# Performance work log

Measured on AMD Instinct MI355X. Metric: run time of the kernel, lower is better.

## Reference

```python
import jax, jax.numpy as jnp
import numpy as np

L = 8192
E = 1024
H = 16
D = E // H  # head_dim = 64


def setup_inputs() -> dict:
    key = jax.random.key(0)
    ks = jax.random.split(key, 5)
    x = jax.random.normal(ks[0], (L, E), dtype=jnp.float32)
    in_proj_weight = jax.random.normal(ks[1], (3 * E, E), dtype=jnp.float32) * (1.0 / np.sqrt(E))
    in_proj_bias = jax.random.normal(ks[2], (3 * E,), dtype=jnp.float32) * 0.02
    out_proj_weight = jax.random.normal(ks[3], (E, E), dtype=jnp.float32) * (1.0 / np.sqrt(E))
    out_proj_bias = jax.random.normal(ks[4], (E,), dtype=jnp.float32) * 0.02
    return {
        "x": x,
        "in_proj_weight": in_proj_weight,
        "in_proj_bias": in_proj_bias,
        "out_proj_weight": out_proj_weight,
        "out_proj_bias": out_proj_bias,
    }


def reference(x, in_proj_weight, in_proj_bias, out_proj_weight, out_proj_bias):
    # Single-token query (decode-style): q from x[:1], k/v from full sequence.
    q = x[:1] @ in_proj_weight[:E].T + in_proj_bias[:E]            # [1, E]
    k = x @ in_proj_weight[E:2 * E].T + in_proj_bias[E:2 * E]      # [L, E]
    v = x @ in_proj_weight[2 * E:].T + in_proj_bias[2 * E:]        # [L, E]

    q = q.reshape(1, H, D).transpose(1, 0, 2)   # [H, 1, D]
    k = k.reshape(L, H, D).transpose(1, 2, 0)   # [H, D, L]
    v = v.reshape(L, H, D).transpose(1, 0, 2)   # [H, L, D]

    scale = 1.0 / np.sqrt(D).astype(np.float32)
    dot = jnp.matmul(q, k) * scale              # [H, 1, L]
    attn = jax.nn.softmax(dot, axis=-1)
    out = jnp.matmul(attn, v)                   # [H, 1, D]
    out = out.transpose(1, 0, 2).reshape(1, E)  # [1, E]
    return out @ out_proj_weight.T + out_proj_bias
```

## Files before the change

### kernel.cpp

```cpp
#include <hip/hip_runtime.h>

#define LSEQ 8192
#define E 1024
#define H 16

typedef __attribute__((ext_vector_type(8))) short short8;
typedef __attribute__((ext_vector_type(4))) float f32x4;

__device__ inline unsigned short f2bf(float f) {
    union { float f; unsigned int i; } v; v.f = f;
    unsigned int x = v.i;
    return (unsigned short)((x + 0x7fffu + ((x >> 16) & 1u)) >> 16);
}

__device__ inline float wave_reduce_sum(float v) {
    #pragma unroll
    for (int off = 32; off > 0; off >>= 1) v += __shfl_xor(v, off, 64);
    return v;
}

__global__ __launch_bounds__(256) void k0_q(
    const float* __restrict__ x, const float* __restrict__ W,
    const float* __restrict__ bias, float* __restrict__ q_ws,
    float* __restrict__ S_ws)
{
    if (blockIdx.x == 0 && threadIdx.x < 16) S_ws[threadIdx.x] = 0.f;
    int wave = threadIdx.x >> 6, lane = threadIdx.x & 63;
    int i = blockIdx.x * 4 + wave;
    const f32x4* wp = (const f32x4*)(W + i * E) + lane * 4;
    const f32x4* xp = (const f32x4*)(x) + lane * 4;
    float s = 0.f;
    #pragma unroll
    for (int j = 0; j < 4; j++) {
        f32x4 w4 = wp[j], x4 = xp[j];
        s += w4[0]*x4[0] + w4[1]*x4[1] + w4[2]*x4[2] + w4[3]*x4[3];
    }
    s = wave_reduce_sum(s);
    if (lane == 0) q_ws[i] = s + bias[i];
}

__global__ __launch_bounds__(256) void k1_rc(
    const float* __restrict__ W, const float* __restrict__ bias,
    const float* __restrict__ q_ws, unsigned short* __restrict__ r_bf,
    float* __restrict__ c_ws)
{
    __shared__ float red[4][64];
    int hb = blockIdx.x >> 4, ec = blockIdx.x & 15;
    int lane = threadIdx.x & 63, wq = threadIdx.x >> 6;
    int e = ec * 64 + lane;
    const float* qh = q_ws + hb * 64;
    float acc = 0.f;
    #pragma unroll
    for (int i = 0; i < 16; i++) {
        int d = wq * 16 + i;
        acc += qh[d] * W[(E + hb * 64 + d) * E + e];
    }
    red[wq][lane] = acc;
    __syncthreads();
    if (wq == 0) {
        float s = red[0][lane] + red[1][lane] + red[2][lane] + red[3][lane];
        r_bf[hb * E + e] = f2bf(s * 0.125f);
    }
    if (ec == 0 && wq == 1) {
        float v = qh[lane] * bias[E + hb * 64 + lane];
        v = wave_reduce_sum(v);
        if (lane == 0) c_ws[hb] = v * 0.125f;
    }
}

__global__ __launch_bounds__(512, 1) void k2_fused(
    const float* __restrict__ x,
    const unsigned short* __restrict__ r_bf,
    const float* __restrict__ c_ws,
    float* __restrict__ partial, float* __restrict__ S_ws)
{
    __shared__ float x_lds[16 * 1028];
    __shared__ float sp[8 * 64 * 4];
    __shared__ float p_lds[16 * 16];
    __shared__ float esum[16];

    const int tid  = threadIdx.x;
    const int wave = tid >> 6, lane = tid & 63;
    const int beta = blockIdx.x;

    if (tid < 16) esum[tid] = 0.f;
    float acc[32];
    #pragma unroll
    for (int i = 0; i < 32; i++) acc[i] = 0.f;
    int lbase = beta * 32;

    for (int t = 0; t < 2; t++) {
        int R0 = lbase + t * 16;
        __syncthreads();
        {
            int row = tid >> 5, ch = tid & 31;
            const f32x4* src = (const f32x4*)(x + (R0 + row) * E);
            float* dst = x_lds + row * 1028;
            #pragma unroll
            for (int j = 0; j < 8; j++) {
                int c4 = ch + 32 * j;
                *(f32x4*)(dst + c4 * 4) = src[c4];
            }
        }
        __syncthreads();
        {
            int rw = lane & 15, quad = lane >> 4;
            f32x4 sacc = {0.f, 0.f, 0.f, 0.f};
            const float* arow = x_lds + rw * 1028 + wave * 128 + quad * 8;
            const short8* bp = (const short8*)(r_bf + rw * E + wave * 128 + quad * 8);
            #pragma unroll
            for (int kk = 0; kk < 4; kk++) {
                f32x4 a0 = *(const f32x4*)(arow + kk * 32);
                f32x4 a1 = *(const f32x4*)(arow + kk * 32 + 4);
                short8 af;
                af[0] = (short)f2bf(a0[0]); af[1] = (short)f2bf(a0[1]);
                af[2] = (short)f2bf(a0[2]); af[3] = (short)f2bf(a0[3]);
                af[4] = (short)f2bf(a1[0]); af[5] = (short)f2bf(a1[1]);
                af[6] = (short)f2bf(a1[2]); af[7] = (short)f2bf(a1[3]);
                short8 bfr = bp[kk * 4];
                sacc = __builtin_amdgcn_mfma_f32_16x16x32_bf16(af, bfr, sacc, 0, 0, 0);
            }
            *(f32x4*)&sp[(wave * 64 + lane) * 4] = sacc;
        }
        __syncthreads();
        if (tid < 256) {
            int m = tid >> 4, h = tid & 15;
            int ln = (m >> 2) * 16 + h, rg = m & 3;
            float s = c_ws[h];
            #pragma unroll
            for (int w = 0; w < 8; w++) s += sp[(w * 64 + ln) * 4 + rg];
            float p = __expf(s);
            p_lds[m * 16 + h] = p;
            atomicAdd(&esum[h], p);
        }
        __syncthreads();
        #pragma unroll 4
        for (int m = 0; m < 16; m++) {
            float2 xv = *(const float2*)&x_lds[m * 1028 + tid * 2];
            const f32x4* pp = (const f32x4*)&p_lds[m * 16];
            #pragma unroll
            for (int g = 0; g < 4; g++) {
                f32x4 pv = pp[g];
                acc[(g * 4 + 0) * 2 + 0] += pv[0] * xv.x;
                acc[(g * 4 + 0) * 2 + 1] += pv[0] * xv.y;
                acc[(g * 4 + 1) * 2 + 0] += pv[1] * xv.x;
                acc[(g * 4 + 1) * 2 + 1] += pv[1] * xv.y;
                acc[(g * 4 + 2) * 2 + 0] += pv[2] * xv.x;
                acc[(g * 4 + 2) * 2 + 1] += pv[2] * xv.y;
                acc[(g * 4 + 3) * 2 + 0] += pv[3] * xv.x;
                acc[(g * 4 + 3) * 2 + 1] += pv[3] * xv.y;
            }
        }
    }
    __syncthreads();
    #pragma unroll
    for (int h = 0; h < 16; h++) {
        float2 v; v.x = acc[h * 2]; v.y = acc[h * 2 + 1];
        *(float2*)&partial[(beta * 16 + h) * E + tid * 2] = v;
    }
    if (tid < 16) atomicAdd(&S_ws[tid], esum[tid]);
}

__global__ __launch_bounds__(512) void k3_reduce(
    const float* __restrict__ partial, float* __restrict__ u_ws)
{
    __shared__ float red[8 * 64];
    int wave = threadIdx.x >> 6, lane = threadIdx.x & 63;
    int o = blockIdx.x * 64 + lane;
    float s = 0.f;
    for (int bb = wave; bb < 256; bb += 8) s += partial[bb * (H * E) + o];
    red[wave * 64 + lane] = s;
    __syncthreads();
    if (wave == 0) {
        float tot = 0.f;
        #pragma unroll
        for (int w = 0; w < 8; w++) tot += red[w * 64 + lane];
        u_ws[o] = tot;
    }
}

__global__ __launch_bounds__(256) void k4_oh(
    const float* __restrict__ W, const float* __restrict__ bias,
    const float* __restrict__ u_ws, const float* __restrict__ S_ws,
    float* __restrict__ oh_ws)
{
    int wave = threadIdx.x >> 6, lane = threadIdx.x & 63;
    int i = blockIdx.x * 4 + wave;
    int h = i >> 6;
    const f32x4* wp = (const f32x4*)(W + (2 * E + i) * E) + lane * 4;
    const f32x4* up = (const f32x4*)(u_ws + h * E) + lane * 4;
    float s = 0.f;
    #pragma unroll
    for (int j = 0; j < 4; j++) {
        f32x4 w4 = wp[j], u4 = up[j];
        s += w4[0]*u4[0] + w4[1]*u4[1] + w4[2]*u4[2] + w4[3]*u4[3];
    }
    s = wave_reduce_sum(s);
    if (lane == 0) oh_ws[i] = s / S_ws[h] + bias[2 * E + i];
}

__global__ __launch_bounds__(256) void k5_out(
    const float* __restrict__ Wout, const float* __restrict__ bout,
    const float* __restrict__ oh_ws, float* __restrict__ out)
{
    int wave = threadIdx.x >> 6, lane = threadIdx.x & 63;
    int j = blockIdx.x * 4 + wave;
    const f32x4* wp = (const f32x4*)(Wout + j * E) + lane * 4;
    const f32x4* op = (const f32x4*)(oh_ws) + lane * 4;
    float s = 0.f;
    #pragma unroll
    for (int jj = 0; jj < 4; jj++) {
        f32x4 w4 = wp[jj], o4 = op[jj];
        s += w4[0]*o4[0] + w4[1]*o4[1] + w4[2]*o4[2] + w4[3]*o4[3];
    }
    s = wave_reduce_sum(s);
    if (lane == 0) out[j] = s + bout[j];
}

extern "C" void kernel_launch(void* const* d_in, const int* in_sizes, int n_in,
                              void* d_out, int out_size, void* d_ws, size_t ws_size,
                              hipStream_t stream) {
    const float* x  = (const float*)d_in[0];
    const float* W  = (const float*)d_in[1];
    const float* b  = (const float*)d_in[2];
    const float* Wo = (const float*)d_in[3];
    const float* bo = (const float*)d_in[4];
    float* out = (float*)d_out;
    char* ws = (char*)d_ws;

    float* q_ws  = (float*)(ws);
    float* c_ws  = (float*)(ws + 4096);
    float* S_ws  = (float*)(ws + 4224);
    float* oh_ws = (float*)(ws + 4352);
    unsigned short* r_bf = (unsigned short*)(ws + 8448);
    float* u_ws  = (float*)(ws + 41216);
    float* partial = (float*)(ws + 106752);

    hipLaunchKernelGGL(k0_q,     dim3(256), dim3(256), 0, stream, x, W, b, q_ws, S_ws);
    hipLaunchKernelGGL(k1_rc,    dim3(256), dim3(256), 0, stream, W, b, q_ws, r_bf, c_ws);
    hipLaunchKernelGGL(k2_fused, dim3(256), dim3(512), 0, stream, x, r_bf, c_ws, partial, S_ws);
    hipLaunchKernelGGL(k3_reduce,dim3(256), dim3(512), 0, stream, partial, u_ws);
    hipLaunchKernelGGL(k4_oh,    dim3(256), dim3(256), 0, stream, W, b, u_ws, S_ws, oh_ws);
    hipLaunchKernelGGL(k5_out,   dim3(256), dim3(256), 0, stream, Wo, bo, oh_ws, out);
}
```

Baseline: 119.9 us.

## Fuse q and r projections, shard partial sums with atomics, drop reduce kernel

Merges the q projection and the r/c computation into one kernel, where each block recomputes its head's q in shared memory. The separate reduce kernel is removed: the fused attention kernel now atomically accumulates its partials into 16 shards, and the oh kernel sums those shards. This goes from six launches to four and cuts the partial-buffer traffic from 256 slices to 16. In exchange, q is computed redundantly (16x per head), global float atomics contend across 16 blocks per shard, and the float summation order becomes nondeterministic.

```diff
diff --git a/kernel.cpp b/kernel.cpp
--- a/kernel.cpp
+++ b/kernel.cpp
@@ -3,6 +3,7 @@
 #define LSEQ 8192
 #define E 1024
 #define H 16
+#define NSHARD 16
 
 typedef __attribute__((ext_vector_type(8))) short short8;
 typedef __attribute__((ext_vector_type(4))) float f32x4;
@@ -19,52 +20,62 @@
     return v;
 }
 
-__global__ __launch_bounds__(256) void k0_q(
+__global__ __launch_bounds__(256) void kA_qrc(
     const float* __restrict__ x, const float* __restrict__ W,
-    const float* __restrict__ bias, float* __restrict__ q_ws,
-    float* __restrict__ S_ws)
-{
-    if (blockIdx.x == 0 && threadIdx.x < 16) S_ws[threadIdx.x] = 0.f;
-    int wave = threadIdx.x >> 6, lane = threadIdx.x & 63;
-    int i = blockIdx.x * 4 + wave;
-    const f32x4* wp = (const f32x4*)(W + i * E) + lane * 4;
-    const f32x4* xp = (const f32x4*)(x) + lane * 4;
-    float s = 0.f;
-    #pragma unroll
-    for (int j = 0; j < 4; j++) {
-        f32x4 w4 = wp[j], x4 = xp[j];
-        s += w4[0]*x4[0] + w4[1]*x4[1] + w4[2]*x4[2] + w4[3]*x4[3];
-    }
-    s = wave_reduce_sum(s);
-    if (lane == 0) q_ws[i] = s + bias[i];
-}
-
-__global__ __launch_bounds__(256) void k1_rc(
-    const float* __restrict__ W, const float* __restrict__ bias,
-    const float* __restrict__ q_ws, unsigned short* __restrict__ r_bf,
-    float* __restrict__ c_ws)
-{
+    const float* __restrict__ b, unsigned short* __restrict__ r_bf,
+    float* __restrict__ c_ws, float* __restrict__ partial,
+    float* __restrict__ S_shard)
+{
+    __shared__ float q_lds[64];
     __shared__ float red[4][64];
-    int hb = blockIdx.x >> 4, ec = blockIdx.x & 15;
-    int lane = threadIdx.x & 63, wq = threadIdx.x >> 6;
-    int e = ec * 64 + lane;
-    const float* qh = q_ws + hb * 64;
-    float acc = 0.f;
-    #pragma unroll
-    for (int i = 0; i < 16; i++) {
-        int d = wq * 16 + i;
-        acc += qh[d] * W[(E + hb * 64 + d) * E + e];
-    }
-    red[wq][lane] = acc;
+    const int beta = blockIdx.x;
+    const int h = beta & 15, ec = beta >> 4;
+    const int tid = threadIdx.x;
+    const int wave = tid >> 6, lane = tid & 63;
+
+    {
+        f32x4 z = {0.f, 0.f, 0.f, 0.f};
+        ((f32x4*)partial)[beta * 256 + tid] = z;
+        if (beta == 0) S_shard[tid] = 0.f;
+    }
+
+    {
+        const f32x4* xp = (const f32x4*)(x) + lane * 4;
+        f32x4 x0 = xp[0], x1 = xp[1], x2 = xp[2], x3 = xp[3];
+        #pragma unroll 4
+        for (int i = 0; i < 16; i++) {
+            int d = wave * 16 + i;
+            const f32x4* wp = (const f32x4*)(W + (h * 64 + d) * E) + lane * 4;
+            f32x4 w0 = wp[0], w1 = wp[1], w2 = wp[2], w3 = wp[3];
+            float s = w0[0]*x0[0] + w0[1]*x0[1] + w0[2]*x0[2] + w0[3]*x0[3]
+                    + w1[0]*x1[0] + w1[1]*x1[1] + w1[2]*x1[2] + w1[3]*x1[3]
+                    + w2[0]*x2[0] + w2[1]*x2[1] + w2[2]*x2[2] + w2[3]*x2[3]
+                    + w3[0]*x3[0] + w3[1]*x3[1] + w3[2]*x3[2] + w3[3]*x3[3];
+            s = wave_reduce_sum(s);
+            if (lane == 0) q_lds[d] = s + b[h * 64 + d];
+        }
+    }
     __syncthreads();
-    if (wq == 0) {
-        float s = red[0][lane] + red[1][lane] + red[2][lane] + red[3][lane];
-        r_bf[hb * E + e] = f2bf(s * 0.125f);
-    }
-    if (ec == 0 && wq == 1) {
-        float v = qh[lane] * bias[E + hb * 64 + lane];
-        v = wave_reduce_sum(v);
-        if (lane == 0) c_ws[hb] = v * 0.125f;
+
+    {
+        int e = ec * 64 + lane;
+        float acc = 0.f;
+        #pragma unroll
+        for (int i = 0; i < 16; i++) {
+            int d = wave * 16 + i;
+            acc += q_lds[d] * W[(E + h * 64 + d) * E + e];
+        }
+        red[wave][lane] = acc;
+        __syncthreads();
+        if (wave == 0) {
+            float s = red[0][lane] + red[1][lane] + red[2][lane] + red[3][lane];
+            r_bf[h * E + e] = f2bf(s * 0.125f);
+        }
+        if (ec == 0 && wave == 1) {
+            float v = q_lds[lane] * b[E + h * 64 + lane];
+            v = wave_reduce_sum(v);
+            if (lane == 0) c_ws[h] = v * 0.125f;
+        }
     }
 }
 
@@ -72,7 +83,7 @@
     const float* __restrict__ x,
     const unsigned short* __restrict__ r_bf,
     const float* __restrict__ c_ws,
-    float* __restrict__ partial, float* __restrict__ S_ws)
+    float* __restrict__ partial, float* __restrict__ S_shard)
 {
     __shared__ float x_lds[16 * 1028];
     __shared__ float sp[8 * 64 * 4];
@@ -124,14 +135,14 @@
         }
         __syncthreads();
         if (tid < 256) {
-            int m = tid >> 4, h = tid & 15;
-            int ln = (m >> 2) * 16 + h, rg = m & 3;
-            float s = c_ws[h];
+            int m = tid >> 4, hh = tid & 15;
+            int ln = (m >> 2) * 16 + hh, rg = m & 3;
+            float s = c_ws[hh];
             #pragma unroll
             for (int w = 0; w < 8; w++) s += sp[(w * 64 + ln) * 4 + rg];
             float p = __expf(s);
-            p_lds[m * 16 + h] = p;
-            atomicAdd(&esum[h], p);
+            p_lds[m * 16 + hh] = p;
+            atomicAdd(&esum[hh], p);
         }
         __syncthreads();
         #pragma unroll 4
@@ -153,50 +164,49 @@
         }
     }
     __syncthreads();
-    #pragma unroll
-    for (int h = 0; h < 16; h++) {
-        float2 v; v.x = acc[h * 2]; v.y = acc[h * 2 + 1];
-        *(float2*)&partial[(beta * 16 + h) * E + tid * 2] = v;
-    }
-    if (tid < 16) atomicAdd(&S_ws[tid], esum[tid]);
-}
-
-__global__ __launch_bounds__(512) void k3_reduce(
-    const float* __restrict__ partial, float* __restrict__ u_ws)
-{
-    __shared__ float red[8 * 64];
-    int wave = threadIdx.x >> 6, lane = threadIdx.x & 63;
-    int o = blockIdx.x * 64 + lane;
-    float s = 0.f;
-    for (int bb = wave; bb < 256; bb += 8) s += partial[bb * (H * E) + o];
-    red[wave * 64 + lane] = s;
-    __syncthreads();
-    if (wave == 0) {
-        float tot = 0.f;
+    {
+        float* pb = partial + (beta & 15) * (H * E);
         #pragma unroll
-        for (int w = 0; w < 8; w++) tot += red[w * 64 + lane];
-        u_ws[o] = tot;
+        for (int h = 0; h < 16; h++) {
+            atomicAdd(&pb[h * E + tid * 2],     acc[h * 2]);
+            atomicAdd(&pb[h * E + tid * 2 + 1], acc[h * 2 + 1]);
+        }
+        if (tid < 16) atomicAdd(&S_shard[(beta & 15) * 16 + tid], esum[tid]);
     }
 }
 
 __global__ __launch_bounds__(256) void k4_oh(
     const float* __restrict__ W, const float* __restrict__ bias,
-    const float* __restrict__ u_ws, const float* __restrict__ S_ws,
+    const float* __restrict__ partial, const float* __restrict__ S_shard,
     float* __restrict__ oh_ws)
 {
-    int wave = threadIdx.x >> 6, lane = threadIdx.x & 63;
+    __shared__ float u_lds[1024];
+    const int tid = threadIdx.x;
+    const int wave = tid >> 6, lane = tid & 63;
+    const int h = blockIdx.x >> 4;
+
+    for (int e = tid; e < 1024; e += 256) {
+        float s = 0.f;
+        #pragma unroll
+        for (int sh = 0; sh < NSHARD; sh++) s += partial[sh * (H * E) + h * E + e];
+        u_lds[e] = s;
+    }
+    float Sh = 0.f;
+    #pragma unroll
+    for (int sh = 0; sh < NSHARD; sh++) Sh += S_shard[sh * 16 + h];
+    __syncthreads();
+
     int i = blockIdx.x * 4 + wave;
-    int h = i >> 6;
-    const f32x4* wp = (const f32x4*)(W + (2 * E + i) * E) + lane * 4;
-    const f32x4* up = (const f32x4*)(u_ws + h * E) + lane * 4;
+    const f32x4* wp = (const f32x4*)(W + (2 * E + i) * E);
+    const f32x4* up = (const f32x4*)u_lds;
     float s = 0.f;
     #pragma unroll
     for (int j = 0; j < 4; j++) {
-        f32x4 w4 = wp[j], u4 = up[j];
+        f32x4 w4 = wp[j * 64 + lane], u4 = up[j * 64 + lane];
         s += w4[0]*u4[0] + w4[1]*u4[1] + w4[2]*u4[2] + w4[3]*u4[3];
     }
     s = wave_reduce_sum(s);
-    if (lane == 0) oh_ws[i] = s / S_ws[h] + bias[2 * E + i];
+    if (lane == 0) oh_ws[i] = s / Sh + bias[2 * E + i];
 }
 
 __global__ __launch_bounds__(256) void k5_out(
@@ -228,18 +238,18 @@
     float* out = (float*)d_out;
     char* ws = (char*)d_ws;
 
-    float* q_ws  = (float*)(ws);
-    float* c_ws  = (float*)(ws + 4096);
-    float* S_ws  = (float*)(ws + 4224);
-    float* oh_ws = (float*)(ws + 4352);
-    unsigned short* r_bf = (unsigned short*)(ws + 8448);
-    float* u_ws  = (float*)(ws + 41216);
-    float* partial = (float*)(ws + 106752);
-
-    hipLaunchKernelGGL(k0_q,     dim3(256), dim3(256), 0, stream, x, W, b, q_ws, S_ws);
-    hipLaunchKernelGGL(k1_rc,    dim3(256), dim3(256), 0, stream, W, b, q_ws, r_bf, c_ws);
-    hipLaunchKernelGGL(k2_fused, dim3(256), dim3(512), 0, stream, x, r_bf, c_ws, partial, S_ws);
-    hipLaunchKernelGGL(k3_reduce,dim3(256), dim3(512), 0, stream, partial, u_ws);
-    hipLaunchKernelGGL(k4_oh,    dim3(256), dim3(256), 0, stream, W, b, u_ws, S_ws, oh_ws);
-    hipLaunchKernelGGL(k5_out,   dim3(256), dim3(256), 0, stream, Wo, bo, oh_ws, out);
-}
+    float* c_ws    = (float*)(ws);
+    float* S_shard = (float*)(ws + 1024);
+    float* oh_ws   = (float*)(ws + 4096);
+    unsigned short* r_bf = (unsigned short*)(ws + 8192);
+    float* partial = (float*)(ws + 65536);
+
+    hipLaunchKernelGGL(kA_qrc,  dim3(256), dim3(256), 0, stream,
+                       x, W, b, r_bf, c_ws, partial, S_shard);
+    hipLaunchKernelGGL(k2_fused, dim3(256), dim3(512), 0, stream,
+                       x, r_bf, c_ws, partial, S_shard);
+    hipLaunchKernelGGL(k4_oh,   dim3(256), dim3(256), 0, stream,
+                       W, b, partial, S_shard, oh_ws);
+    hipLaunchKernelGGL(k5_out,  dim3(256), dim3(256), 0, stream,
+                       Wo, bo, oh_ws, out);
+}
```

Measured after the change: 142.6 us. 1.19x slower.
